# Optimization experiments

Measured on AMD Instinct MI355X. Metric: run time of the kernel, lower is better.

## Reference

```python
import jax, jax.numpy as jnp
import numpy as np

NUM_HEADS = 8
CHUNK = 64          # dialtion / chunck_size
EPS = 1e-5          # InstanceNorm1d eps
NEG = -1e9


def setup_inputs() -> dict:
    key = jax.random.key(0)
    ks = jax.random.split(key, 8)
    N, C, T = 4, 512, 4096
    x = jax.random.normal(ks[0], (N, C, T), dtype=jnp.float32)
    q = jax.random.normal(ks[1], (N, C, T), dtype=jnp.float32)
    k = jax.random.normal(ks[2], (N, C, T), dtype=jnp.float32)
    v = jax.random.normal(ks[3], (N, C, T), dtype=jnp.float32)
    masks = jnp.ones((N, 1, T), dtype=jnp.float32)
    s = 1.0 / np.sqrt(C)
    W_in = jax.random.normal(ks[4], (3 * C, C), dtype=jnp.float32) * s   # packed q/k/v in-proj
    b_in = jnp.zeros((3 * C,), dtype=jnp.float32)
    W_out = jax.random.normal(ks[5], (C, C), dtype=jnp.float32) * s     # out-proj
    b_out = jnp.zeros((C,), dtype=jnp.float32)
    return {"x": x, "q": q, "k": k, "v": v, "masks": masks,
            "W_in": W_in, "b_in": b_in, "W_out": W_out, "b_out": b_out}


def _chunk_attn(q, k, v, masks, W_in, b_in, W_out, b_out):
    # q,k,v: [N, C, T]; masks: [N, 1, T]
    N, C, T = q.shape
    H, Dh = NUM_HEADS, C // NUM_HEADS
    nc = T // CHUNK
    Wq, Wk, Wv = jnp.split(W_in, 3, axis=0)
    bq, bk, bv = jnp.split(b_in, 3, axis=0)

    def proj(t, W, b):
        # [N,C,T] -> chunked heads [N, nc, CHUNK, H, Dh]
        t = t.transpose(0, 2, 1) @ W.T + b            # [N, T, C]
        return t.reshape(N, nc, CHUNK, H, Dh)

    qh = proj(q, Wq, bq)
    kh = proj(k, Wk, bk)
    vh = proj(v, Wv, bv)

    scale = 1.0 / jnp.sqrt(jnp.asarray(Dh, q.dtype))
    # intra-chunk scores: [N, nc, H, CHUNK, CHUNK]
    scores = jnp.einsum('bnqhd,bnkhd->bnhqk', qh, kh) * scale
    km = masks[:, 0, :].reshape(N, nc, CHUNK)         # key validity per chunk
    scores = scores + jnp.where(km[:, :, None, None, :] > 0, 0.0, NEG)
    attn = jax.nn.softmax(scores, axis=-1)
    out = jnp.einsum('bnhqk,bnkhd->bnqhd', attn, vh).reshape(N, T, C)
    out = out @ W_out.T + b_out                        # [N, T, C]
    out = out.transpose(0, 2, 1) * masks               # [N, C, T], re-mask
    return out


def reference(x, q, k, v, masks, W_in, b_in, W_out, b_out):
    out = _chunk_attn(q, k, v, masks, W_in, b_in, W_out, b_out) + x
    # InstanceNorm1d (affine=False): normalize each (n, c) row over T
    mu = jnp.mean(out, axis=2, keepdims=True)
    var = jnp.mean(jnp.square(out - mu), axis=2, keepdims=True)
    return (out - mu) * jax.lax.rsqrt(var + EPS)
```

## Files before the change

### kernel.cpp

```cpp
#include <hip/hip_runtime.h>
#include <hip/hip_bf16.h>

#define NB 4
#define CC 512
#define TT 4096
#define C3 1536
#define CQK 1024
#define NTC (NB*TT*CC)

typedef __attribute__((ext_vector_type(4))) float f32x4;
typedef __attribute__((ext_vector_type(8))) short short8;
typedef unsigned short ushort;
typedef __attribute__((ext_vector_type(8))) ushort u16x8;

__device__ __forceinline__ ushort f2bf(float f){
    union { float f; unsigned u; } x; x.f = f;
    unsigned r = x.u + 0x7fffu + ((x.u >> 16) & 1u);
    return (ushort)(r >> 16);
}

__device__ __forceinline__ ushort2 pk2bf(float a, float b){
    float2 f2; f2.x = a; f2.y = b;
    __hip_bfloat162 h = __float22bfloat162_rn(f2);
    union { __hip_bfloat162 h2; ushort2 u2; } u; u.h2 = h;
    return u.u2;
}

__device__ __forceinline__ void gload16(const void* g, void* l){
    __builtin_amdgcn_global_load_lds((const __attribute__((address_space(1))) void*)g,
                                     (__attribute__((address_space(3))) void*)l,
                                     16, 0, 0);
}

__global__ __launch_bounds__(256) void prep(const float* __restrict__ q,
                                            const float* __restrict__ k,
                                            const float* __restrict__ v,
                                            const float* __restrict__ Wi,
                                            const float* __restrict__ Wo,
                                            ushort* __restrict__ XT,
                                            ushort* __restrict__ Wb,
                                            ushort* __restrict__ Wob){
    const int tid = threadIdx.x;
    int b = blockIdx.x;
    if (b >= 3072){
        int idx0 = (b - 3072) * 1024 + tid;
        for (int i = 0; i < 4; ++i){
            int idx = idx0 + i*256;
            const float* src; ushort* dst; int j;
            if (idx < 196608){ src = Wi; dst = Wb;  j = idx; }
            else             { src = Wo; dst = Wob; j = idx - 196608; }
            f32x4 vv = *((const f32x4*)src + j);
            ushort4 o;
            *(ushort2*)&o.x = pk2bf(vv[0], vv[1]);
            *(ushort2*)&o.z = pk2bf(vv[2], vv[3]);
            *((ushort4*)dst + j) = o;
        }
        return;
    }
    int tq  = b & 31;
    int cch = (b >> 5) & 7;
    int n   = (b >> 8) & 3;
    int which = b >> 10;
    const float* src = (which == 0) ? q : (which == 1) ? k : v;
    const int c0   = (tid & 7) * 8;
    const int trel = (tid >> 3) * 4;
    const float* base = src + (size_t)n*CC*TT + (size_t)(cch*64 + c0)*TT + (size_t)tq*128 + trel;

    f32x4 cur[8];
    #pragma unroll
    for (int j = 0; j < 8; ++j)
        cur[j] = *(const f32x4*)(base + (size_t)j*TT);

    ushort* dst = XT + (size_t)which*NTC
                + ((size_t)n*TT + (size_t)tq*128 + trel)*CC + cch*64 + c0;
    #pragma unroll
    for (int tj = 0; tj < 4; ++tj){
        u16x8 o;
        #pragma unroll
        for (int j = 0; j < 8; j += 2){
            ushort2 p = pk2bf(cur[j][tj], cur[j+1][tj]);
            o[j] = p.x; o[j+1] = p.y;
        }
        *(u16x8*)(dst + (size_t)tj*CC) = o;
    }
}

__global__ __launch_bounds__(256) void proj_gemm(const ushort* __restrict__ XT,
                                                 const ushort* __restrict__ Wb,
                                                 const float* __restrict__ b_in,
                                                 ushort* __restrict__ P,
                                                 ushort* __restrict__ Vt){
    __shared__ __align__(16) ushort smem[128*136];
    ushort* sA = smem;
    ushort* sB = smem + 128*64;
    const int tid = threadIdx.x;
    const int bid = blockIdx.x;
    const int mtile  = ((bid & 7) << 4) | ((bid >> 3) & 15);
    const int cotile = bid >> 7;
    const int co0 = cotile * 128;
    const int m0  = mtile * 128;
    const int which = co0 >> 9;
    const ushort* Abase = XT + (size_t)which*NTC + (size_t)m0*CC;
    const ushort* Bbase = Wb + (size_t)co0*CC;
    const int w = tid >> 6, lane = tid & 63;
    const int wr = w >> 1, wc = w & 1;
    const int l15 = lane & 15, quad = lane >> 4;

    const ushort* gA[4]; const ushort* gB[4];
    ushort* lA[4]; ushort* lB[4];
    for (int i = 0; i < 4; ++i){
        int slot = i*256 + tid;
        int m = slot >> 3, k8 = slot & 7, kk = k8 ^ (m & 7);
        gA[i] = Abase + (size_t)m*CC + kk*8;
        gB[i] = Bbase + (size_t)m*CC + kk*8;
        int lbase = (i*256 + (tid & ~63)) * 8;
        lA[i] = sA + lbase;  lB[i] = sB + lbase;
    }

    f32x4 acc[4][4] = {};
    for (int kb = 0; kb < 8; ++kb){
        __syncthreads();
        for (int i = 0; i < 4; ++i){
            gload16(gA[i] + kb*64, lA[i]);
            gload16(gB[i] + kb*64, lB[i]);
        }
        __syncthreads();
        for (int ks = 0; ks < 2; ++ks){
            short8 aF[4], bF[4];
            for (int mi = 0; mi < 4; ++mi){
                int m = wr*64 + mi*16 + l15;
                aF[mi] = *(const short8*)&sA[(m*8 + ((ks*4 + quad) ^ (m & 7)))*8];
            }
            for (int ni = 0; ni < 4; ++ni){
                int m = wc*64 + ni*16 + l15;
                bF[ni] = *(const short8*)&sB[(m*8 + ((ks*4 + quad) ^ (m & 7)))*8];
            }
            for (int mi = 0; mi < 4; ++mi)
                for (int ni = 0; ni < 4; ++ni)
                    acc[mi][ni] = __builtin_amdgcn_mfma_f32_16x16x32_bf16(
                        aF[mi], bF[ni], acc[mi][ni], 0, 0, 0);
        }
    }

    float bj[4];
    for (int ni = 0; ni < 4; ++ni) bj[ni] = b_in[co0 + wc*64 + ni*16 + l15];

    __syncthreads();
    ushort* sOut = smem;
    if (which < 2){
        for (int mi = 0; mi < 4; ++mi){
            int mrow = wr*64 + mi*16 + quad*4;
            for (int ni = 0; ni < 4; ++ni){
                int col = wc*64 + ni*16 + l15;
                for (int r = 0; r < 4; ++r)
                    sOut[(mrow + r)*136 + col] = f2bf(acc[mi][ni][r] + bj[ni]);
            }
        }
    } else {
        for (int mi = 0; mi < 4; ++mi){
            int mrow = wr*64 + mi*16 + quad*4;
            for (int ni = 0; ni < 4; ++ni){
                int col = wc*64 + ni*16 + l15;
                for (int r = 0; r < 4; ++r)
                    sOut[col*136 + mrow + r] = f2bf(acc[mi][ni][r] + bj[ni]);
            }
        }
    }
    __syncthreads();
    if (which < 2){
        for (int i = 0; i < 8; ++i){
            int flat = i*256 + tid;
            int row = flat >> 4, cs = (flat & 15)*8;
            u16x8 val = *(const u16x8*)&sOut[row*136 + cs];
            *(u16x8*)(P + (size_t)(m0 + row)*CQK + which*512 + (co0 & 511) + cs) = val;
        }
    } else {
        int n = m0 >> 12, t0 = m0 & 4095;
        for (int i = 0; i < 8; ++i){
            int flat = i*256 + tid;
            int row = flat >> 4, cs = (flat & 15)*8;
            int cl = (co0 - 1024) + row;
            int h = cl >> 6, d = cl & 63;
            u16x8 val = *(const u16x8*)&sOut[row*136 + cs];
            *(u16x8*)(Vt + (((size_t)n*8 + h)*64 + d)*TT + t0 + cs) = val;
        }
    }
}

__global__ __launch_bounds__(256) void attn_kernel(const ushort* __restrict__ P,
                                                   const ushort* __restrict__ Vt,
                                                   const float* __restrict__ masks,
                                                   ushort* __restrict__ ctx){
    __shared__ __align__(16) ushort sQ[64*64], sK[64*64], sV[64*64];
    __shared__ __align__(16) ushort sP[64][72];
    __shared__ __align__(16) ushort sO[64*72];
    int bid = blockIdx.x;
    int h = bid & 7, ch = (bid >> 3) & 63, n = bid >> 9;
    const int tid = threadIdx.x, lane = tid & 63, w = tid >> 6;
    const int l15 = lane & 15, quad = lane >> 4;
    const size_t rowbase = (size_t)n*TT + (size_t)ch*64;
    for (int i = 0; i < 2; ++i){
        int slot = i*256 + tid;
        int r = slot >> 3, k8 = slot & 7, kk = k8 ^ (r & 7);
        int lbase = (i*256 + (tid & ~63)) * 8;
        const ushort* gq = P + (rowbase + r)*CQK + h*64 + kk*8;
        gload16(gq,        sQ + lbase);
        gload16(gq + 512,  sK + lbase);
        const ushort* gv = Vt + (((size_t)n*8 + h)*64 + r)*TT + ch*64 + kk*8;
        gload16(gv,        sV + lbase);
    }
    __syncthreads();
    const int m0w = w*16;
    short8 aQ[2]; f32x4 accS[4] = {};
    for (int ks = 0; ks < 2; ++ks){
        int m = m0w + l15;
        aQ[ks] = *(const short8*)&sQ[(m*8 + ((ks*4 + quad) ^ (m & 7)))*8];
    }
    for (int ni = 0; ni < 4; ++ni)
        for (int ks = 0; ks < 2; ++ks){
            int m = ni*16 + l15;
            short8 bK = *(const short8*)&sK[(m*8 + ((ks*4 + quad) ^ (m & 7)))*8];
            accS[ni] = __builtin_amdgcn_mfma_f32_16x16x32_bf16(aQ[ks], bK, accS[ni], 0,0,0);
        }
    float madd[4];
    for (int ni = 0; ni < 4; ++ni){
        float mv = masks[(size_t)n*TT + ch*64 + ni*16 + l15];
        madd[ni] = (mv > 0.f) ? 0.f : -1e9f;
    }
    float s[4][4];
    for (int ni = 0; ni < 4; ++ni)
        for (int r = 0; r < 4; ++r) s[ni][r] = accS[ni][r]*0.125f + madd[ni];
    float ex[4][4];
    for (int r = 0; r < 4; ++r){
        float m1 = fmaxf(fmaxf(s[0][r], s[1][r]), fmaxf(s[2][r], s[3][r]));
        for (int d = 1; d < 16; d <<= 1) m1 = fmaxf(m1, __shfl_xor(m1, d));
        float a = 0.f;
        for (int ni = 0; ni < 4; ++ni){ float e = __expf(s[ni][r] - m1); ex[ni][r] = e; a += e; }
        for (int d = 1; d < 16; d <<= 1) a += __shfl_xor(a, d);
        float rs = 1.0f / a;
        for (int ni = 0; ni < 4; ++ni)
            sP[m0w + quad*4 + r][ni*16 + l15] = f2bf(ex[ni][r] * rs);
    }
    short8 aP[2]; f32x4 accO[4] = {};
    for (int ks = 0; ks < 2; ++ks)
        aP[ks] = *(const short8*)&sP[m0w + l15][ks*32 + quad*8];
    for (int ni = 0; ni < 4; ++ni)
        for (int ks = 0; ks < 2; ++ks){
            int m = ni*16 + l15;
            short8 bV = *(const short8*)&sV[(m*8 + ((ks*4 + quad) ^ (m & 7)))*8];
            accO[ni] = __builtin_amdgcn_mfma_f32_16x16x32_bf16(aP[ks], bV, accO[ni], 0,0,0);
        }
    for (int ni = 0; ni < 4; ++ni)
        for (int r = 0; r < 4; ++r)
            sO[(m0w + quad*4 + r)*72 + ni*16 + l15] = f2bf(accO[ni][r]);
    __syncthreads();
    for (int i = 0; i < 2; ++i){
        int flat = i*256 + tid;
        int row = flat >> 3, cs = (flat & 7)*8;
        u16x8 val = *(const u16x8*)&sO[row*72 + cs];
        *(u16x8*)(ctx + (rowbase + row)*CC + h*64 + cs) = val;
    }
}

__global__ __launch_bounds__(256) void out_gemm(const ushort* __restrict__ ctx,
                                                const ushort* __restrict__ Wob,
                                                const float* __restrict__ b_out,
                                                const float* __restrict__ x,
                                                const float* __restrict__ masks,
                                                float* __restrict__ out){
    __shared__ __align__(16) ushort smem[16896];
    ushort* sA = smem;
    ushort* sB = smem + 128*64;
    float* fOut = (float*)smem;
    const int tid = threadIdx.x;
    const int bid = blockIdx.x;
    const int mtile  = ((bid & 7) << 4) | ((bid >> 3) & 15);
    const int cotile = bid >> 7;
    const int co0 = cotile * 64;
    const int m0  = mtile * 128;
    const int n = m0 >> 12, t0 = m0 & 4095;
    const ushort* Abase = ctx + (size_t)m0*CC;
    const ushort* Bbase = Wob + (size_t)co0*CC;
    const int w = tid >> 6, lane = tid & 63;
    const int wr = w >> 1, wc = w & 1;
    const int l15 = lane & 15, quad = lane >> 4;

    const ushort* gA[4]; ushort* lA[4];
    const ushort* gB[2]; ushort* lB[2];
    for (int i = 0; i < 4; ++i){
        int slot = i*256 + tid;
        int m = slot >> 3, k8 = slot & 7, kk = k8 ^ (m & 7);
        gA[i] = Abase + (size_t)m*CC + kk*8;
        lA[i] = sA + (i*256 + (tid & ~63)) * 8;
    }
    for (int i = 0; i < 2; ++i){
        int slot = i*256 + tid;
        int m = slot >> 3, k8 = slot & 7, kk = k8 ^ (m & 7);
        gB[i] = Bbase + (size_t)m*CC + kk*8;
        lB[i] = sB + (i*256 + (tid & ~63)) * 8;
    }

    f32x4 acc[4][2] = {};
    for (int kb = 0; kb < 8; ++kb){
        __syncthreads();
        for (int i = 0; i < 4; ++i) gload16(gA[i] + kb*64, lA[i]);
        for (int i = 0; i < 2; ++i) gload16(gB[i] + kb*64, lB[i]);
        __syncthreads();
        for (int ks = 0; ks < 2; ++ks){
            short8 aF[4], bF[2];
            for (int mi = 0; mi < 4; ++mi){
                int m = wr*64 + mi*16 + l15;
                aF[mi] = *(const short8*)&sA[(m*8 + ((ks*4 + quad) ^ (m & 7)))*8];
            }
            for (int ni = 0; ni < 2; ++ni){
                int m = wc*32 + ni*16 + l15;
                bF[ni] = *(const short8*)&sB[(m*8 + ((ks*4 + quad) ^ (m & 7)))*8];
            }
            for (int mi = 0; mi < 4; ++mi)
                for (int ni = 0; ni < 2; ++ni)
                    acc[mi][ni] = __builtin_amdgcn_mfma_f32_16x16x32_bf16(
                        aF[mi], bF[ni], acc[mi][ni], 0, 0, 0);
        }
    }
    float bo[2];
    for (int ni = 0; ni < 2; ++ni) bo[ni] = b_out[co0 + wc*32 + ni*16 + l15];

    __syncthreads();
    for (int mi = 0; mi < 4; ++mi){
        int tl = wr*64 + mi*16 + quad*4;
        for (int ni = 0; ni < 2; ++ni){
            int cl = wc*32 + ni*16 + l15;
            f32x4 vv;
            for (int r = 0; r < 4; ++r) vv[r] = acc[mi][ni][r] + bo[ni];
            *(f32x4*)&fOut[cl*132 + tl] = vv;
        }
    }
    __syncthreads();
    for (int i = 0; i < 8; ++i){
        int flat = i*256 + tid;
        int co = flat >> 5, ts = (flat & 31)*4;
        f32x4 a = *(const f32x4*)&fOut[co*132 + ts];
        f32x4 mk = *(const f32x4*)(masks + (size_t)n*TT + t0 + ts);
        f32x4 xv = *(const f32x4*)(x + ((size_t)n*CC + co0 + co)*TT + t0 + ts);
        f32x4 o;
        for (int r = 0; r < 4; ++r) o[r] = a[r]*mk[r] + xv[r];
        *(f32x4*)(out + ((size_t)n*CC + co0 + co)*TT + t0 + ts) = o;
    }
}

__global__ __launch_bounds__(256) void inorm(float* __restrict__ out){
    __shared__ float sS[4], sQ2[4];
    float* row = out + (size_t)blockIdx.x * TT;
    f32x4 vbuf[4];
    float s = 0.f, ss = 0.f;
    for (int i = 0; i < 4; ++i){
        f32x4 vv = *(const f32x4*)(row + (size_t)(i*256 + threadIdx.x)*4);
        vbuf[i] = vv;
        for (int r = 0; r < 4; ++r){ s += vv[r]; ss += vv[r]*vv[r]; }
    }
    for (int d = 1; d < 64; d <<= 1){ s += __shfl_xor(s, d); ss += __shfl_xor(ss, d); }
    int w = threadIdx.x >> 6;
    if ((threadIdx.x & 63) == 0){ sS[w] = s; sQ2[w] = ss; }
    __syncthreads();
    s  = sS[0] + sS[1] + sS[2] + sS[3];
    ss = sQ2[0] + sQ2[1] + sQ2[2] + sQ2[3];
    float mean = s * (1.0f/TT);
    float var  = ss * (1.0f/TT) - mean*mean;
    float rstd = rsqrtf(var + 1e-5f);
    for (int i = 0; i < 4; ++i){
        f32x4 vv = vbuf[i], o;
        for (int r = 0; r < 4; ++r) o[r] = (vv[r] - mean) * rstd;
        *(f32x4*)(row + (size_t)(i*256 + threadIdx.x)*4) = o;
    }
}

extern "C" void kernel_launch(void* const* d_in, const int* in_sizes, int n_in,
                              void* d_out, int out_size, void* d_ws, size_t ws_size,
                              hipStream_t stream) {
    const float* x     = (const float*)d_in[0];
    const float* q     = (const float*)d_in[1];
    const float* k     = (const float*)d_in[2];
    const float* v     = (const float*)d_in[3];
    const float* masks = (const float*)d_in[4];
    const float* W_in  = (const float*)d_in[5];
    const float* b_in  = (const float*)d_in[6];
    const float* W_out = (const float*)d_in[7];
    const float* b_out = (const float*)d_in[8];
    float* out = (float*)d_out;

    ushort* ws  = (ushort*)d_ws;
    ushort* XT  = ws;
    ushort* Wb  = ws + (size_t)3*NTC;
    ushort* Wob = Wb + 786432;
    ushort* P   = Wob + 262144;
    ushort* Vt  = P + (size_t)NB*TT*CQK;
    ushort* ctx = ws;

    prep<<<3328, 256, 0, stream>>>(q, k, v, W_in, W_out, XT, Wb, Wob);
    proj_gemm<<<1536, 256, 0, stream>>>(XT, Wb, b_in, P, Vt);
    attn_kernel<<<2048, 256, 0, stream>>>(P, Vt, masks, ctx);
    out_gemm<<<1024, 256, 0, stream>>>(ctx, Wob, b_out, x, masks, out);
    inorm<<<2048, 256, 0, stream>>>(out);
}
```

Measured before the change: 255.3 us.

## Fuse q/k/v transpose and bf16 conversion into projection GEMM A-tile load

```diff
diff --git a/kernel.cpp b/kernel.cpp
--- a/kernel.cpp
+++ b/kernel.cpp
@@ -32,60 +32,31 @@
                                      16, 0, 0);
 }
 
-__global__ __launch_bounds__(256) void prep(const float* __restrict__ q,
-                                            const float* __restrict__ k,
-                                            const float* __restrict__ v,
-                                            const float* __restrict__ Wi,
+__device__ __forceinline__ int apos(int m, int cb){
+    return (m*8 + ((cb + m + (m >> 3)) & 7))*8;
+}
+
+__global__ __launch_bounds__(256) void wcvt(const float* __restrict__ Wi,
                                             const float* __restrict__ Wo,
-                                            ushort* __restrict__ XT,
                                             ushort* __restrict__ Wb,
                                             ushort* __restrict__ Wob){
-    const int tid = threadIdx.x;
-    int b = blockIdx.x;
-    if (b >= 3072){
-        int idx0 = (b - 3072) * 1024 + tid;
-        for (int i = 0; i < 4; ++i){
-            int idx = idx0 + i*256;
-            const float* src; ushort* dst; int j;
-            if (idx < 196608){ src = Wi; dst = Wb;  j = idx; }
-            else             { src = Wo; dst = Wob; j = idx - 196608; }
-            f32x4 vv = *((const f32x4*)src + j);
-            ushort4 o;
-            *(ushort2*)&o.x = pk2bf(vv[0], vv[1]);
-            *(ushort2*)&o.z = pk2bf(vv[2], vv[3]);
-            *((ushort4*)dst + j) = o;
-        }
-        return;
-    }
-    int tq  = b & 31;
-    int cch = (b >> 5) & 7;
-    int n   = (b >> 8) & 3;
-    int which = b >> 10;
-    const float* src = (which == 0) ? q : (which == 1) ? k : v;
-    const int c0   = (tid & 7) * 8;
-    const int trel = (tid >> 3) * 4;
-    const float* base = src + (size_t)n*CC*TT + (size_t)(cch*64 + c0)*TT + (size_t)tq*128 + trel;
-
-    f32x4 cur[8];
-    #pragma unroll
-    for (int j = 0; j < 8; ++j)
-        cur[j] = *(const f32x4*)(base + (size_t)j*TT);
-
-    ushort* dst = XT + (size_t)which*NTC
-                + ((size_t)n*TT + (size_t)tq*128 + trel)*CC + cch*64 + c0;
-    #pragma unroll
-    for (int tj = 0; tj < 4; ++tj){
-        u16x8 o;
-        #pragma unroll
-        for (int j = 0; j < 8; j += 2){
-            ushort2 p = pk2bf(cur[j][tj], cur[j+1][tj]);
-            o[j] = p.x; o[j+1] = p.y;
-        }
-        *(u16x8*)(dst + (size_t)tj*CC) = o;
-    }
-}
-
-__global__ __launch_bounds__(256) void proj_gemm(const ushort* __restrict__ XT,
+    int idx0 = blockIdx.x * 1024 + threadIdx.x;
+    for (int i = 0; i < 4; ++i){
+        int idx = idx0 + i*256;
+        const float* src; ushort* dst; int j;
+        if (idx < 196608){ src = Wi; dst = Wb;  j = idx; }
+        else             { src = Wo; dst = Wob; j = idx - 196608; }
+        f32x4 vv = *((const f32x4*)src + j);
+        ushort4 o;
+        *(ushort2*)&o.x = pk2bf(vv[0], vv[1]);
+        *(ushort2*)&o.z = pk2bf(vv[2], vv[3]);
+        *((ushort4*)dst + j) = o;
+    }
+}
+
+__global__ __launch_bounds__(256) void proj_gemm(const float* __restrict__ q,
+                                                 const float* __restrict__ k,
+                                                 const float* __restrict__ v,
                                                  const ushort* __restrict__ Wb,
                                                  const float* __restrict__ b_in,
                                                  ushort* __restrict__ P,
@@ -100,36 +71,51 @@
     const int co0 = cotile * 128;
     const int m0  = mtile * 128;
     const int which = co0 >> 9;
-    const ushort* Abase = XT + (size_t)which*NTC + (size_t)m0*CC;
+    const float* src = (which == 0) ? q : (which == 1) ? k : v;
+    const int n  = m0 >> 12, t0 = m0 & 4095;
     const ushort* Bbase = Wb + (size_t)co0*CC;
     const int w = tid >> 6, lane = tid & 63;
     const int wr = w >> 1, wc = w & 1;
     const int l15 = lane & 15, quad = lane >> 4;
 
-    const ushort* gA[4]; const ushort* gB[4];
-    ushort* lA[4]; ushort* lB[4];
+    const int cbA = (w << 1) | (lane >> 5);
+    const int tA  = lane & 31;
+    const float* Abase = src + (size_t)n*CC*TT + (size_t)(cbA*8)*TT + t0 + tA*4;
+
+    const ushort* gB[4]; ushort* lB[4];
     for (int i = 0; i < 4; ++i){
         int slot = i*256 + tid;
-        int m = slot >> 3, k8 = slot & 7, kk = k8 ^ (m & 7);
-        gA[i] = Abase + (size_t)m*CC + kk*8;
-        gB[i] = Bbase + (size_t)m*CC + kk*8;
-        int lbase = (i*256 + (tid & ~63)) * 8;
-        lA[i] = sA + lbase;  lB[i] = sB + lbase;
+        int mr = slot >> 3, k8 = slot & 7, kk = k8 ^ (mr & 7);
+        gB[i] = Bbase + (size_t)mr*CC + kk*8;
+        lB[i] = sB + (i*256 + (tid & ~63)) * 8;
     }
 
     f32x4 acc[4][4] = {};
     for (int kb = 0; kb < 8; ++kb){
+        f32x4 cur[8];
+        const float* Ab = Abase + (size_t)(kb*64)*TT;
+        #pragma unroll
+        for (int j = 0; j < 8; ++j)
+            cur[j] = *(const f32x4*)(Ab + (size_t)j*TT);
         __syncthreads();
-        for (int i = 0; i < 4; ++i){
-            gload16(gA[i] + kb*64, lA[i]);
-            gload16(gB[i] + kb*64, lB[i]);
-        }
+        #pragma unroll
+        for (int tj = 0; tj < 4; ++tj){
+            int m = tA*4 + tj;
+            u16x8 o;
+            #pragma unroll
+            for (int j = 0; j < 8; j += 2){
+                ushort2 p = pk2bf(cur[j][tj], cur[j+1][tj]);
+                o[j] = p.x; o[j+1] = p.y;
+            }
+            *(u16x8*)&sA[apos(m, cbA)] = o;
+        }
+        for (int i = 0; i < 4; ++i) gload16(gB[i] + kb*64, lB[i]);
         __syncthreads();
         for (int ks = 0; ks < 2; ++ks){
             short8 aF[4], bF[4];
             for (int mi = 0; mi < 4; ++mi){
                 int m = wr*64 + mi*16 + l15;
-                aF[mi] = *(const short8*)&sA[(m*8 + ((ks*4 + quad) ^ (m & 7)))*8];
+                aF[mi] = *(const short8*)&sA[apos(m, ks*4 + quad)];
             }
             for (int ni = 0; ni < 4; ++ni){
                 int m = wc*64 + ni*16 + l15;
@@ -175,7 +161,6 @@
             *(u16x8*)(P + (size_t)(m0 + row)*CQK + which*512 + (co0 & 511) + cs) = val;
         }
     } else {
-        int n = m0 >> 12, t0 = m0 & 4095;
         for (int i = 0; i < 8; ++i){
             int flat = i*256 + tid;
             int row = flat >> 4, cs = (flat & 15)*8;
@@ -389,15 +374,14 @@
     float* out = (float*)d_out;
 
     ushort* ws  = (ushort*)d_ws;
-    ushort* XT  = ws;
-    ushort* Wb  = ws + (size_t)3*NTC;
+    ushort* ctx = ws;
+    ushort* Wb  = ws + (size_t)NTC;
     ushort* Wob = Wb + 786432;
     ushort* P   = Wob + 262144;
     ushort* Vt  = P + (size_t)NB*TT*CQK;
-    ushort* ctx = ws;
-
-    prep<<<3328, 256, 0, stream>>>(q, k, v, W_in, W_out, XT, Wb, Wob);
-    proj_gemm<<<1536, 256, 0, stream>>>(XT, Wb, b_in, P, Vt);
+
+    wcvt<<<256, 256, 0, stream>>>(W_in, W_out, Wb, Wob);
+    proj_gemm<<<1536, 256, 0, stream>>>(q, k, v, Wb, b_in, P, Vt);
     attn_kernel<<<2048, 256, 0, stream>>>(P, Vt, masks, ctx);
     out_gemm<<<1024, 256, 0, stream>>>(ctx, Wob, b_out, x, masks, out);
     inorm<<<2048, 256, 0, stream>>>(out);
```

Result: faster. 245.1 us (-4.0%).
